# Optimization experiments

Hardware: AMD Instinct MI355X
Metric: run time of the kernel (lower is better)

Reference implementation:

```python
import jax, jax.numpy as jnp
import numpy as np

B, NM, MB, D = 16, 64, 64, 1024
NH, NKV, MEM = 16, 8, 64
HD = D // NH            # 64
S = MB + MEM            # per-step attention length
EPS = 1e-6

def precompute_freqs_cis(dim, end, theta=10000.0):
    freqs = 1.0 / (theta ** (jnp.arange(0, dim, 2)[: dim // 2].astype(jnp.float32) / dim))
    t = jnp.arange(end, dtype=jnp.float32)
    return jnp.exp(1j * jnp.outer(t, freqs))  # [end, dim//2] complex64

def apply_rope(x, fcis):
    # x: [s, h, d], fcis: [s, d//2] complex
    xc = x.reshape(x.shape[0], x.shape[1], HD // 2, 2)
    xc = jax.lax.complex(xc[..., 0], xc[..., 1]) * fcis[:, None, :]
    return jnp.stack([jnp.real(xc), jnp.imag(xc)], axis=-1).reshape(x.shape)

def layer_norm(x, scale, bias):
    m = x.mean(-1, keepdims=True)
    v = x.var(-1, keepdims=True)
    return (x - m) * jax.lax.rsqrt(v + EPS) * scale + bias

def setup_inputs() -> dict:
    key = jax.random.key(0)
    ks = jax.random.split(key, 8)
    s = 1.0 / np.sqrt(D)
    return {
        'hidden_states': jax.random.normal(ks[0], (B, NM, MB, D), jnp.float32),
        'mask': jax.random.bernoulli(ks[1], 0.9, (B, NM)),
        'mem_state': jax.random.normal(ks[2], (MEM, D), jnp.float32) * s,
        'wq': jax.random.normal(ks[3], (D, D), jnp.float32) * s,
        'wk': jax.random.normal(ks[4], (D, NKV * HD), jnp.float32) * s,
        'wv': jax.random.normal(ks[5], (D, NKV * HD), jnp.float32) * s,
        'wo': jax.random.normal(ks[6], (D, D), jnp.float32) * s,
        'pre_scale': jnp.ones((D,), jnp.float32),
        'pre_bias': jnp.zeros((D,), jnp.float32),
        'post_scale': jnp.ones((D,), jnp.float32),
        'post_bias': jnp.zeros((D,), jnp.float32),
    }

def reference(hidden_states, mask, mem_state, wq, wk, wv, wo, pre_scale, pre_bias, post_scale, post_bias):
    fcis = precompute_freqs_cis(HD, S)  # constant RoPE buffer, first S positions used
    rep = NH // NKV
    scale = 1.0 / np.sqrt(HD)

    def step(mem, inp):
        x_mb, m = inp  # x_mb: [MB, D], m: scalar bool
        h = layer_norm(jnp.concatenate([x_mb, mem], axis=0), pre_scale, pre_bias)  # [S, D]
        q = (h @ wq).reshape(S, NH, HD)
        k = (h @ wk).reshape(S, NKV, HD)
        v = (h @ wv).reshape(S, NKV, HD)
        q = apply_rope(q, fcis)
        k = apply_rope(k, fcis)
        k = jnp.repeat(k, rep, axis=1)  # GQA: expand kv heads
        v = jnp.repeat(v, rep, axis=1)
        qb, kb, vb = q.astype(jnp.bfloat16), k.astype(jnp.bfloat16), v.astype(jnp.bfloat16)
        logits = jnp.einsum('qhd,khd->hqk', qb, kb).astype(jnp.float32) * scale
        att = jax.nn.softmax(logits, axis=-1).astype(jnp.bfloat16)
        enc = jnp.einsum('hqk,khd->qhd', att, vb).reshape(S, D).astype(jnp.float32)
        out = enc[-MEM:] @ wo  # only memory-slot queries feed the update
        new_mem = layer_norm(out + mem, post_scale, post_bias)
        new_mem = jnp.where(m, new_mem, mem)  # lax.cond branch as select
        return new_mem, None

    def per_batch(x, m):
        final, _ = jax.lax.scan(step, mem_state, (x, m))
        return final

    return jax.vmap(per_batch)(hidden_states, mask)  # [B, MEM, D]
```

## Files before the change

### kernel.cpp

```cpp
#include <hip/hip_runtime.h>


typedef __attribute__((ext_vector_type(8))) _Float16 f16x8;
typedef __attribute__((ext_vector_type(4))) _Float16 f16x4;
typedef __attribute__((ext_vector_type(8))) short    s16x8;
typedef __attribute__((ext_vector_type(4))) float    f32x4;

#define NB   16
#define NMs  64
#define MBs  64
#define Dm   1024
#define NHh  16
#define NKVh 8
#define HDd  64
#define MEMm 64
#define Sq   128

__device__ __align__(16) _Float16      g_W1t[2048 * 1024];
__device__ __align__(16) _Float16      g_Wot[1024 * 1024];
__device__ __align__(16) float         g_rc[128 * 32];
__device__ __align__(16) float         g_rs[128 * 32];
__device__                unsigned char g_mask[NB * NMs];
__device__ __align__(16) _Float16      g_hx[(size_t)NB * NMs * MBs * Dm];
__device__ __align__(16) _Float16      g_hmem[NB * MEMm * Dm];
__device__ __align__(16) float         g_memA[NB * MEMm * Dm];
__device__ __align__(16) float         g_memB[NB * MEMm * Dm];
__device__ __align__(16) unsigned short g_qb[NB * NHh * 64 * 64];
__device__ __align__(16) unsigned short g_kb[NB * NKVh * 128 * 64];
__device__ __align__(16) unsigned short g_vt[NB * NKVh * 64 * 128];
__device__ __align__(16) _Float16      g_enc[NB * 64 * Dm];
__device__ __align__(16) float         g_outp[NB * 64 * Dm];

__device__ __forceinline__ unsigned short f2bf(float x) {
    union { float f; unsigned u; } v; v.f = x;
    unsigned u = v.u;
    return (unsigned short)((u + 0x7fffu + ((u >> 16) & 1u)) >> 16);
}
__device__ __forceinline__ float bf2f(unsigned short h) {
    union { unsigned u; float f; } v; v.u = ((unsigned)h) << 16; return v.f;
}

__device__ __forceinline__ void block_stats(float s, float ss, float eps,
                                            float* mean, float* rstd) {
    for (int off = 32; off > 0; off >>= 1) {
        s  += __shfl_down(s, off);
        ss += __shfl_down(ss, off);
    }
    __shared__ float red[8];
    int wid = threadIdx.x >> 6, lane = threadIdx.x & 63;
    __syncthreads();
    if (lane == 0) { red[wid] = s; red[4 + wid] = ss; }
    __syncthreads();
    float ts  = red[0] + red[1] + red[2] + red[3];
    float tss = red[4] + red[5] + red[6] + red[7];
    float m   = ts * (1.0f / 1024.0f);
    float var = tss * (1.0f / 1024.0f) - m * m;
    *mean = m;
    *rstd = rsqrtf(var + eps);
}

__global__ void k_transpose(const float* __restrict__ in, int ncols, int dsel) {
    _Float16* out = (dsel == 0) ? g_W1t
                  : (dsel == 1) ? (g_W1t + 1024 * 1024)
                  : (dsel == 2) ? (g_W1t + 1536 * 1024)
                                : g_Wot;
    __shared__ float tile[64][65];
    int bk = blockIdx.x, bn = blockIdx.y;
    int c = threadIdx.x & 63, rg = threadIdx.x >> 6;
    int k0 = bk * 64, n0 = bn * 64;
    for (int i = 0; i < 16; i++) {
        int r = rg * 16 + i;
        tile[r][c] = in[(size_t)(k0 + r) * ncols + n0 + c];
    }
    __syncthreads();
    for (int i = 0; i < 16; i++) {
        int r = rg * 16 + i;
        out[(size_t)(n0 + r) * 1024 + k0 + c] = (_Float16)tile[c][r];
    }
}

__global__ void k_rope() {
    int t = threadIdx.x;
    for (int j = 0; j < 32; j++) {
        double f = pow(10000.0, -(double)j / 32.0);
        double a = (double)t * f;
        g_rc[t * 32 + j] = (float)cos(a);
        g_rs[t * 32 + j] = (float)sin(a);
    }
}

__global__ void k_mask(const unsigned int* __restrict__ ip) {
    __shared__ int byteFmt;
    int t = threadIdx.x;
    if (t == 0) byteFmt = 0;
    __syncthreads();
    if (t < 256) {
        unsigned v = ip[t];
        if (!(v == 0u || v == 1u || v == 0x3F800000u)) byteFmt = 1;
    }
    __syncthreads();
    unsigned char m = byteFmt ? (((const unsigned char*)ip)[t] != 0)
                              : (ip[t] != 0u);
    g_mask[t] = m;
}

__global__ void k_ln_hx(const float* __restrict__ x,
                        const float* __restrict__ sc, const float* __restrict__ bi) {
    size_t row = blockIdx.x;
    int t = threadIdx.x;
    float4 v = ((const float4*)(x + row * 1024))[t];
    float mean, rstd;
    block_stats(v.x + v.y + v.z + v.w,
                v.x * v.x + v.y * v.y + v.z * v.z + v.w * v.w, 1e-6f, &mean, &rstd);
    float4 s4 = ((const float4*)sc)[t];
    float4 b4 = ((const float4*)bi)[t];
    f16x4 o;
    o[0] = (_Float16)((v.x - mean) * rstd * s4.x + b4.x);
    o[1] = (_Float16)((v.y - mean) * rstd * s4.y + b4.y);
    o[2] = (_Float16)((v.z - mean) * rstd * s4.z + b4.z);
    o[3] = (_Float16)((v.w - mean) * rstd * s4.w + b4.w);
    *(f16x4*)(g_hx + row * 1024 + t * 4) = o;
}

__global__ void k_ln_init(const float* __restrict__ ms,
                          const float* __restrict__ sc, const float* __restrict__ bi) {
    int b = blockIdx.x >> 6, r = blockIdx.x & 63;
    int t = threadIdx.x;
    float4 v = ((const float4*)(ms + (size_t)r * 1024))[t];
    ((float4*)(g_memA + ((size_t)b * 64 + r) * 1024))[t] = v;
    float mean, rstd;
    block_stats(v.x + v.y + v.z + v.w,
                v.x * v.x + v.y * v.y + v.z * v.z + v.w * v.w, 1e-6f, &mean, &rstd);
    float4 s4 = ((const float4*)sc)[t];
    float4 b4 = ((const float4*)bi)[t];
    f16x4 o;
    o[0] = (_Float16)((v.x - mean) * rstd * s4.x + b4.x);
    o[1] = (_Float16)((v.y - mean) * rstd * s4.y + b4.y);
    o[2] = (_Float16)((v.z - mean) * rstd * s4.z + b4.z);
    o[3] = (_Float16)((v.w - mean) * rstd * s4.w + b4.w);
    *(f16x4*)(g_hmem + ((size_t)b * 64 + r) * 1024 + t * 4) = o;
}

__device__ __forceinline__ void gemm_core(const _Float16* __restrict__ Abase,
                                          const _Float16* __restrict__ Bbase,
                                          _Float16* As, _Float16* Bs,
                                          f32x4 acc[2][2]) {
    int tid = threadIdx.x;
    int w = tid >> 6, l = tid & 63;
    int mo = (w & 1) * 32, no = (w >> 1) * 32;
    int sr = tid >> 2, sk = (tid & 3) * 8;
    int fr = l & 15, fq = (l >> 4) * 8;
    for (int kt = 0; kt < 32; ++kt) {
        f16x8 av = *(const f16x8*)(Abase + (size_t)sr * 1024 + kt * 32 + sk);
        f16x8 bv = *(const f16x8*)(Bbase + (size_t)sr * 1024 + kt * 32 + sk);
        __syncthreads();
        *(f16x8*)&As[sr * 40 + sk] = av;
        *(f16x8*)&Bs[sr * 40 + sk] = bv;
        __syncthreads();
        f16x8 a0 = *(const f16x8*)&As[(mo + fr) * 40 + fq];
        f16x8 a1 = *(const f16x8*)&As[(mo + 16 + fr) * 40 + fq];
        f16x8 b0 = *(const f16x8*)&Bs[(no + fr) * 40 + fq];
        f16x8 b1 = *(const f16x8*)&Bs[(no + 16 + fr) * 40 + fq];
        acc[0][0] = __builtin_amdgcn_mfma_f32_16x16x32_f16(a0, b0, acc[0][0], 0, 0, 0);
        acc[0][1] = __builtin_amdgcn_mfma_f32_16x16x32_f16(a0, b1, acc[0][1], 0, 0, 0);
        acc[1][0] = __builtin_amdgcn_mfma_f32_16x16x32_f16(a1, b0, acc[1][0], 0, 0, 0);
        acc[1][1] = __builtin_amdgcn_mfma_f32_16x16x32_f16(a1, b1, acc[1][1], 0, 0, 0);
    }
}

__launch_bounds__(256)
__global__ void k_gemm1(int s) {
    int bid = blockIdx.x;
    int b = bid / 48, t48 = bid % 48;
    int mtile = (t48 < 16) ? 0 : 1;
    int ntile = (t48 < 16) ? (16 + t48) : (t48 - 16);
    const _Float16* Abase = (mtile == 0)
        ? (g_hx + ((size_t)(b * NMs + s) * 64) * 1024)
        : (g_hmem + (size_t)b * 64 * 1024);
    const _Float16* Bbase = g_W1t + (size_t)ntile * 64 * 1024;
    __shared__ __align__(16) _Float16 As[64 * 40];
    __shared__ __align__(16) _Float16 Bs[64 * 40];
    f32x4 acc[2][2] = {};
    gemm_core(Abase, Bbase, As, Bs, acc);

    int tid = threadIdx.x, w = tid >> 6, l = tid & 63;
    int mo = (w & 1) * 32, no = (w >> 1) * 32;
    int quad = l >> 4, col = l & 15;
    int m0 = mtile * 64 + mo;
    int n0 = ntile * 64 + no;
    for (int i = 0; i < 2; i++)
        for (int j = 0; j < 2; j++)
            for (int r = 0; r < 4; r++) {
                float val = acc[i][j][r];
                float p = __shfl_xor(val, 1);
                int m = m0 + i * 16 + quad * 4 + r;
                int n = n0 + j * 16 + col;
                int d = n & 63;
                if (ntile < 16) {
                    int jj = d >> 1;
                    float c = g_rc[m * 32 + jj], sn = g_rs[m * 32 + jj];
                    float o = (d & 1) ? (p * sn + val * c) : (val * c - p * sn);
                    g_qb[(((size_t)b * 16 + ntile) * 64 + (m - 64)) * 64 + d] = f2bf(o);
                } else if (ntile < 24) {
                    int kvh = ntile - 16;
                    int jj = d >> 1;
                    float c = g_rc[m * 32 + jj], sn = g_rs[m * 32 + jj];
                    float o = (d & 1) ? (p * sn + val * c) : (val * c - p * sn);
                    g_kb[(((size_t)b * 8 + kvh) * 128 + m) * 64 + d] = f2bf(o);
                } else {
                    int kvh = ntile - 24;
                    g_vt[(((size_t)b * 8 + kvh) * 64 + d) * 128 + m] = f2bf(val);
                }
            }
}

__launch_bounds__(256)
__global__ void k_attn() {
    int b = blockIdx.x >> 4, h = blockIdx.x & 15, kvh = h >> 1;
    int tid = threadIdx.x, w = tid >> 6, l = tid & 63;
    int fr = l & 15, fq = (l >> 4) * 8;
    const unsigned short* qp = g_qb + ((size_t)b * 16 + h) * 64 * 64;
    const unsigned short* kp = g_kb + ((size_t)b * 8 + kvh) * 128 * 64;
    const unsigned short* vp = g_vt + ((size_t)b * 8 + kvh) * 64 * 128;

    s16x8 aq0 = *(const s16x8*)(qp + (w * 16 + fr) * 64 + fq);
    s16x8 aq1 = *(const s16x8*)(qp + (w * 16 + fr) * 64 + 32 + fq);
    f32x4 sc[8];
    for (int nt = 0; nt < 8; nt++) {
        sc[nt] = (f32x4){0.f, 0.f, 0.f, 0.f};
        s16x8 kb0 = *(const s16x8*)(kp + (nt * 16 + fr) * 64 + fq);
        s16x8 kb1 = *(const s16x8*)(kp + (nt * 16 + fr) * 64 + 32 + fq);
        sc[nt] = __builtin_amdgcn_mfma_f32_16x16x32_bf16(aq0, kb0, sc[nt], 0, 0, 0);
        sc[nt] = __builtin_amdgcn_mfma_f32_16x16x32_bf16(aq1, kb1, sc[nt], 0, 0, 0);
    }
    float lv[8][4];
    for (int nt = 0; nt < 8; nt++)
        for (int r = 0; r < 4; r++)
            lv[nt][r] = bf2f(f2bf(sc[nt][r])) * 0.125f;

    int quad = l >> 4;
    __shared__ __align__(16) unsigned short att_s[64 * 136];
    for (int r = 0; r < 4; r++) {
        float mx = -1e30f;
        for (int nt = 0; nt < 8; nt++) mx = fmaxf(mx, lv[nt][r]);
        for (int off = 1; off < 16; off <<= 1) mx = fmaxf(mx, __shfl_xor(mx, off));
        float sm = 0.f;
        for (int nt = 0; nt < 8; nt++) { lv[nt][r] = expf(lv[nt][r] - mx); sm += lv[nt][r]; }
        for (int off = 1; off < 16; off <<= 1) sm += __shfl_xor(sm, off);
        float inv = 1.0f / sm;
        int row = w * 16 + quad * 4 + r;
        for (int nt = 0; nt < 8; nt++)
            att_s[row * 136 + nt * 16 + fr] = f2bf(lv[nt][r] * inv);
    }
    f32x4 o[4];
    for (int nt = 0; nt < 4; nt++) o[nt] = (f32x4){0.f, 0.f, 0.f, 0.f};
    for (int kt = 0; kt < 4; kt++) {
        s16x8 a = *(const s16x8*)&att_s[(w * 16 + fr) * 136 + kt * 32 + fq];
        for (int nt = 0; nt < 4; nt++) {
            s16x8 bv = *(const s16x8*)(vp + (nt * 16 + fr) * 128 + kt * 32 + fq);
            o[nt] = __builtin_amdgcn_mfma_f32_16x16x32_bf16(a, bv, o[nt], 0, 0, 0);
        }
    }
    for (int nt = 0; nt < 4; nt++)
        for (int r = 0; r < 4; r++) {
            int m = w * 16 + quad * 4 + r;
            int d = nt * 16 + fr;
            g_enc[((size_t)b * 64 + m) * 1024 + h * 64 + d] =
                (_Float16)bf2f(f2bf(o[nt][r]));
        }
}

__launch_bounds__(256)
__global__ void k_gemm2() {
    int b = blockIdx.x >> 4, ntile = blockIdx.x & 15;
    const _Float16* Abase = g_enc + (size_t)b * 64 * 1024;
    const _Float16* Bbase = g_Wot + (size_t)ntile * 64 * 1024;
    __shared__ __align__(16) _Float16 As[64 * 40];
    __shared__ __align__(16) _Float16 Bs[64 * 40];
    f32x4 acc[2][2] = {};
    gemm_core(Abase, Bbase, As, Bs, acc);

    int tid = threadIdx.x, w = tid >> 6, l = tid & 63;
    int mo = (w & 1) * 32, no = (w >> 1) * 32;
    int quad = l >> 4, col = l & 15;
    for (int i = 0; i < 2; i++)
        for (int j = 0; j < 2; j++)
            for (int r = 0; r < 4; r++) {
                int m = mo + i * 16 + quad * 4 + r;
                int n = ntile * 64 + no + j * 16 + col;
                g_outp[((size_t)b * 64 + m) * 1024 + n] = acc[i][j][r];
            }
}

__global__ void k_ln2(int s, float* __restrict__ dout,
                      const float* __restrict__ psc, const float* __restrict__ pbi,
                      const float* __restrict__ qsc, const float* __restrict__ qbi) {
    int b = blockIdx.x >> 6, r = blockIdx.x & 63;
    const float* memIn = (s & 1) ? g_memB : g_memA;
    float* memOut = (s == 63) ? dout : ((s & 1) ? g_memA : g_memB);
    int t = threadIdx.x;
    size_t row = (size_t)b * 64 + r;
    float4 ov = ((const float4*)(g_outp + row * 1024))[t];
    float4 mv = ((const float4*)(memIn + row * 1024))[t];
    float4 y = {ov.x + mv.x, ov.y + mv.y, ov.z + mv.z, ov.w + mv.w};
    float mean, rstd;
    block_stats(y.x + y.y + y.z + y.w,
                y.x * y.x + y.y * y.y + y.z * y.z + y.w * y.w, 1e-6f, &mean, &rstd);
    float4 s4 = ((const float4*)psc)[t];
    float4 b4 = ((const float4*)pbi)[t];
    float4 nm = {(y.x - mean) * rstd * s4.x + b4.x,
                 (y.y - mean) * rstd * s4.y + b4.y,
                 (y.z - mean) * rstd * s4.z + b4.z,
                 (y.w - mean) * rstd * s4.w + b4.w};
    int mk = g_mask[b * 64 + s];
    float4 sel = mk ? nm : mv;
    ((float4*)(memOut + row * 1024))[t] = sel;
    float m2, rs2;
    block_stats(sel.x + sel.y + sel.z + sel.w,
                sel.x * sel.x + sel.y * sel.y + sel.z * sel.z + sel.w * sel.w,
                1e-6f, &m2, &rs2);
    float4 c4 = ((const float4*)qsc)[t];
    float4 d4 = ((const float4*)qbi)[t];
    f16x4 o;
    o[0] = (_Float16)((sel.x - m2) * rs2 * c4.x + d4.x);
    o[1] = (_Float16)((sel.y - m2) * rs2 * c4.y + d4.y);
    o[2] = (_Float16)((sel.z - m2) * rs2 * c4.z + d4.z);
    o[3] = (_Float16)((sel.w - m2) * rs2 * c4.w + d4.w);
    *(f16x4*)(g_hmem + row * 1024 + t * 4) = o;
}

extern "C" void kernel_launch(void* const* d_in, const int* in_sizes, int n_in,
                              void* d_out, int out_size, void* d_ws, size_t ws_size,
                              hipStream_t stream) {
    (void)in_sizes; (void)n_in; (void)d_ws; (void)ws_size; (void)out_size;
    const float* hidden    = (const float*)d_in[0];
    const unsigned int* mk = (const unsigned int*)d_in[1];
    const float* mem_state = (const float*)d_in[2];
    const float* wq  = (const float*)d_in[3];
    const float* wk  = (const float*)d_in[4];
    const float* wv  = (const float*)d_in[5];
    const float* wo  = (const float*)d_in[6];
    const float* pre_s  = (const float*)d_in[7];
    const float* pre_b  = (const float*)d_in[8];
    const float* post_s = (const float*)d_in[9];
    const float* post_b = (const float*)d_in[10];
    float* out = (float*)d_out;

    k_transpose<<<dim3(16, 16), 256, 0, stream>>>(wq, 1024, 0);
    k_transpose<<<dim3(16, 8),  256, 0, stream>>>(wk, 512, 1);
    k_transpose<<<dim3(16, 8),  256, 0, stream>>>(wv, 512, 2);
    k_transpose<<<dim3(16, 16), 256, 0, stream>>>(wo, 1024, 3);
    k_rope<<<1, 128, 0, stream>>>();
    k_mask<<<1, 1024, 0, stream>>>(mk);
    k_ln_hx<<<NB * NMs * MBs, 256, 0, stream>>>(hidden, pre_s, pre_b);
    k_ln_init<<<NB * MEMm, 256, 0, stream>>>(mem_state, pre_s, pre_b);

    for (int s = 0; s < NMs; ++s) {
        k_gemm1<<<NB * 48, 256, 0, stream>>>(s);
        k_attn<<<NB * NHh, 256, 0, stream>>>();
        k_gemm2<<<NB * 16, 256, 0, stream>>>();
        k_ln2<<<NB * MEMm, 256, 0, stream>>>(s, out, post_s, post_b, pre_s, pre_b);
    }
}
```

Before: 4.094 ms.

## Precompute hidden-state K/V projections in one batched GEMM and fuse QKV projection with attention

```diff
diff --git a/kernel.cpp b/kernel.cpp
--- a/kernel.cpp
+++ b/kernel.cpp
@@ -14,7 +14,6 @@
 #define NKVh 8
 #define HDd  64
 #define MEMm 64
-#define Sq   128
 
 __device__ __align__(16) _Float16      g_W1t[2048 * 1024];
 __device__ __align__(16) _Float16      g_Wot[1024 * 1024];
@@ -25,9 +24,8 @@
 __device__ __align__(16) _Float16      g_hmem[NB * MEMm * Dm];
 __device__ __align__(16) float         g_memA[NB * MEMm * Dm];
 __device__ __align__(16) float         g_memB[NB * MEMm * Dm];
-__device__ __align__(16) unsigned short g_qb[NB * NHh * 64 * 64];
-__device__ __align__(16) unsigned short g_kb[NB * NKVh * 128 * 64];
-__device__ __align__(16) unsigned short g_vt[NB * NKVh * 64 * 128];
+__device__ __align__(16) unsigned short g_kx[(size_t)NMs * NB * NKVh * 64 * 64];
+__device__ __align__(16) unsigned short g_vx[(size_t)NMs * NB * NKVh * 64 * 64];
 __device__ __align__(16) _Float16      g_enc[NB * 64 * Dm];
 __device__ __align__(16) float         g_outp[NB * 64 * Dm];
 
@@ -38,6 +36,12 @@
 }
 __device__ __forceinline__ float bf2f(unsigned short h) {
     union { unsigned u; float f; } v; v.u = ((unsigned)h) << 16; return v.f;
+}
+
+__device__ __forceinline__ void gload_lds16(const void* g, void* l) {
+    __builtin_amdgcn_global_load_lds(
+        (const __attribute__((address_space(1))) unsigned int*)g,
+        (__attribute__((address_space(3))) unsigned int*)l, 16, 0, 0);
 }
 
 __device__ __forceinline__ void block_stats(float s, float ss, float eps,
@@ -141,127 +145,219 @@
     *(f16x4*)(g_hmem + ((size_t)b * 64 + r) * 1024 + t * 4) = o;
 }
 
-__device__ __forceinline__ void gemm_core(const _Float16* __restrict__ Abase,
-                                          const _Float16* __restrict__ Bbase,
-                                          _Float16* As, _Float16* Bs,
-                                          f32x4 acc[2][2]) {
-    int tid = threadIdx.x;
-    int w = tid >> 6, l = tid & 63;
-    int mo = (w & 1) * 32, no = (w >> 1) * 32;
-    int sr = tid >> 2, sk = (tid & 3) * 8;
-    int fr = l & 15, fq = (l >> 4) * 8;
+__launch_bounds__(256)
+__global__ void k_kvx() {
+    int tm = blockIdx.x, tn = blockIdx.y;
+    int tid = threadIdx.x, w = tid >> 6, l = tid & 63;
+    int fr = l & 15, kc = l >> 4;
+    __shared__ __align__(16) _Float16 As[8 * 512];
+    __shared__ __align__(16) _Float16 Bs[8 * 512];
+    __shared__ __align__(16) unsigned short Ct[128 * 132];
+    const _Float16* A = g_hx + (size_t)tm * 128 * 1024;
+    const _Float16* B = g_W1t + (size_t)(1024 + tn * 128) * 1024;
+    int wm = w & 1, wn = w >> 1;
+    f32x4 acc[4][4];
+    #pragma unroll
+    for (int i = 0; i < 4; i++)
+        #pragma unroll
+        for (int j = 0; j < 4; j++) acc[i][j] = (f32x4){0.f, 0.f, 0.f, 0.f};
+
     for (int kt = 0; kt < 32; ++kt) {
-        f16x8 av = *(const f16x8*)(Abase + (size_t)sr * 1024 + kt * 32 + sk);
-        f16x8 bv = *(const f16x8*)(Bbase + (size_t)sr * 1024 + kt * 32 + sk);
-        __syncthreads();
-        *(f16x8*)&As[sr * 40 + sk] = av;
-        *(f16x8*)&Bs[sr * 40 + sk] = bv;
-        __syncthreads();
-        f16x8 a0 = *(const f16x8*)&As[(mo + fr) * 40 + fq];
-        f16x8 a1 = *(const f16x8*)&As[(mo + 16 + fr) * 40 + fq];
-        f16x8 b0 = *(const f16x8*)&Bs[(no + fr) * 40 + fq];
-        f16x8 b1 = *(const f16x8*)&Bs[(no + 16 + fr) * 40 + fq];
-        acc[0][0] = __builtin_amdgcn_mfma_f32_16x16x32_f16(a0, b0, acc[0][0], 0, 0, 0);
-        acc[0][1] = __builtin_amdgcn_mfma_f32_16x16x32_f16(a0, b1, acc[0][1], 0, 0, 0);
-        acc[1][0] = __builtin_amdgcn_mfma_f32_16x16x32_f16(a1, b0, acc[1][0], 0, 0, 0);
-        acc[1][1] = __builtin_amdgcn_mfma_f32_16x16x32_f16(a1, b1, acc[1][1], 0, 0, 0);
-    }
-}
-
-__launch_bounds__(256)
-__global__ void k_gemm1(int s) {
-    int bid = blockIdx.x;
-    int b = bid / 48, t48 = bid % 48;
-    int mtile = (t48 < 16) ? 0 : 1;
-    int ntile = (t48 < 16) ? (16 + t48) : (t48 - 16);
-    const _Float16* Abase = (mtile == 0)
-        ? (g_hx + ((size_t)(b * NMs + s) * 64) * 1024)
-        : (g_hmem + (size_t)b * 64 * 1024);
-    const _Float16* Bbase = g_W1t + (size_t)ntile * 64 * 1024;
-    __shared__ __align__(16) _Float16 As[64 * 40];
-    __shared__ __align__(16) _Float16 Bs[64 * 40];
-    f32x4 acc[2][2] = {};
-    gemm_core(Abase, Bbase, As, Bs, acc);
-
-    int tid = threadIdx.x, w = tid >> 6, l = tid & 63;
-    int mo = (w & 1) * 32, no = (w >> 1) * 32;
-    int quad = l >> 4, col = l & 15;
-    int m0 = mtile * 64 + mo;
-    int n0 = ntile * 64 + no;
-    for (int i = 0; i < 2; i++)
-        for (int j = 0; j < 2; j++)
+        #pragma unroll
+        for (int jj = 0; jj < 2; ++jj) {
+            int rg = w * 2 + jj;
+            gload_lds16(A + (size_t)(rg * 16 + fr) * 1024 + kt * 32 + kc * 8,
+                        (char*)As + rg * 1024);
+            gload_lds16(B + (size_t)(rg * 16 + fr) * 1024 + kt * 32 + kc * 8,
+                        (char*)Bs + rg * 1024);
+        }
+        __syncthreads();
+        f16x8 af[4], bg[4];
+        #pragma unroll
+        for (int i = 0; i < 4; i++) {
+            af[i] = *(const f16x8*)&As[(wm * 4 + i) * 512 + kc * 128 + fr * 8];
+            bg[i] = *(const f16x8*)&Bs[(wn * 4 + i) * 512 + kc * 128 + fr * 8];
+        }
+        #pragma unroll
+        for (int i = 0; i < 4; i++)
+            #pragma unroll
+            for (int j = 0; j < 4; j++)
+                acc[i][j] = __builtin_amdgcn_mfma_f32_16x16x32_f16(af[i], bg[j], acc[i][j], 0, 0, 0);
+        __syncthreads();
+    }
+    int quad = kc;
+    #pragma unroll
+    for (int i = 0; i < 4; i++)
+        #pragma unroll
+        for (int j = 0; j < 4; j++)
+            #pragma unroll
             for (int r = 0; r < 4; r++) {
                 float val = acc[i][j][r];
                 float p = __shfl_xor(val, 1);
-                int m = m0 + i * 16 + quad * 4 + r;
-                int n = n0 + j * 16 + col;
-                int d = n & 63;
-                if (ntile < 16) {
-                    int jj = d >> 1;
-                    float c = g_rc[m * 32 + jj], sn = g_rs[m * 32 + jj];
-                    float o = (d & 1) ? (p * sn + val * c) : (val * c - p * sn);
-                    g_qb[(((size_t)b * 16 + ntile) * 64 + (m - 64)) * 64 + d] = f2bf(o);
-                } else if (ntile < 24) {
-                    int kvh = ntile - 16;
-                    int jj = d >> 1;
-                    float c = g_rc[m * 32 + jj], sn = g_rs[m * 32 + jj];
-                    float o = (d & 1) ? (p * sn + val * c) : (val * c - p * sn);
-                    g_kb[(((size_t)b * 8 + kvh) * 128 + m) * 64 + d] = f2bf(o);
+                int rl = wm * 64 + i * 16 + quad * 4 + r;
+                int cl = wn * 64 + j * 16 + fr;
+                int c = tn * 128 + cl;
+                unsigned short ob;
+                if (c < 512) {
+                    int d = c & 63, pos = rl & 63;
+                    int j2 = d >> 1;
+                    float cc = g_rc[pos * 32 + j2], sn = g_rs[pos * 32 + j2];
+                    float o = (d & 1) ? (p * sn + val * cc) : (val * cc - p * sn);
+                    ob = f2bf(o);
                 } else {
-                    int kvh = ntile - 24;
-                    g_vt[(((size_t)b * 8 + kvh) * 64 + d) * 128 + m] = f2bf(val);
+                    ob = f2bf(val);
                 }
+                Ct[rl * 132 + cl] = ob;
             }
+    __syncthreads();
+    int row = tid >> 1, half = tid & 1;
+    size_t R = (size_t)tm * 128 + row;
+    int bb = (int)(R >> 12), ss = (int)((R >> 6) & 63), pos = (int)(R & 63);
+    int cb = tn * 128 + half * 64;
+    unsigned short* dst = (cb < 512)
+        ? (g_kx + ((((size_t)ss * 16 + bb) * 8) + (cb >> 6)) * 4096 + pos * 64)
+        : (g_vx + ((((size_t)ss * 16 + bb) * 8) + ((cb - 512) >> 6)) * 4096 + pos * 64);
+    const ushort4* src = (const ushort4*)&Ct[row * 132 + half * 64];
+    #pragma unroll
+    for (int j = 0; j < 16; j++) ((ushort4*)dst)[j] = src[j];
 }
 
 __launch_bounds__(256)
-__global__ void k_attn() {
+__global__ void k_step1(int s) {
     int b = blockIdx.x >> 4, h = blockIdx.x & 15, kvh = h >> 1;
     int tid = threadIdx.x, w = tid >> 6, l = tid & 63;
-    int fr = l & 15, fq = (l >> 4) * 8;
-    const unsigned short* qp = g_qb + ((size_t)b * 16 + h) * 64 * 64;
-    const unsigned short* kp = g_kb + ((size_t)b * 8 + kvh) * 128 * 64;
-    const unsigned short* vp = g_vt + ((size_t)b * 8 + kvh) * 64 * 128;
-
-    s16x8 aq0 = *(const s16x8*)(qp + (w * 16 + fr) * 64 + fq);
-    s16x8 aq1 = *(const s16x8*)(qp + (w * 16 + fr) * 64 + 32 + fq);
+    int fr = l & 15, kc = l >> 4, quad = kc;
+    __shared__ __align__(16) _Float16       Bs[24 * 512];
+    __shared__ __align__(16) unsigned short q_s[64 * 72];
+    __shared__ __align__(16) unsigned short k_s[64 * 72];
+    __shared__ __align__(16) unsigned short vt_s[64 * 136];
+    __shared__ __align__(16) unsigned short p_s[4][16 * 136];
+
+    const _Float16* A = g_hmem + (size_t)b * 64 * 1024;
+
+    {
+        const unsigned short* vx = g_vx + (((size_t)s * 16 + b) * 8 + kvh) * 4096;
+        int pos = tid & 63, dg = tid >> 6;
+        const ushort2* src = (const ushort2*)(vx + pos * 64 + dg * 16);
+        ushort2 tmp[8];
+        #pragma unroll
+        for (int j = 0; j < 8; j++) tmp[j] = src[j];
+        #pragma unroll
+        for (int j = 0; j < 8; j++) {
+            vt_s[(dg * 16 + 2 * j)     * 136 + pos] = tmp[j].x;
+            vt_s[(dg * 16 + 2 * j + 1) * 136 + pos] = tmp[j].y;
+        }
+    }
+
+    f32x4 acc[12];
+    #pragma unroll
+    for (int i = 0; i < 12; i++) acc[i] = (f32x4){0.f, 0.f, 0.f, 0.f};
+    int browQ = h * 64, browK = 1024 + kvh * 64, browV = 1536 + kvh * 64;
+
+    for (int kt = 0; kt < 16; ++kt) {
+        #pragma unroll
+        for (int jj = 0; jj < 6; ++jj) {
+            int m = w * 6 + jj, rg = m % 12, khalf = m / 12;
+            int r192 = rg * 16 + fr;
+            int brow = (r192 < 64) ? (browQ + r192)
+                     : (r192 < 128) ? (browK + r192 - 64)
+                                    : (browV + r192 - 128);
+            gload_lds16(g_W1t + (size_t)brow * 1024 + kt * 64 + khalf * 32 + kc * 8,
+                        (char*)Bs + m * 1024);
+        }
+        f16x8 a0 = *(const f16x8*)(A + (size_t)(w * 16 + fr) * 1024 + kt * 64 + kc * 8);
+        f16x8 a1 = *(const f16x8*)(A + (size_t)(w * 16 + fr) * 1024 + kt * 64 + 32 + kc * 8);
+        __syncthreads();
+        #pragma unroll
+        for (int nt = 0; nt < 12; ++nt) {
+            f16x8 b0 = *(const f16x8*)&Bs[nt * 512 + kc * 128 + fr * 8];
+            f16x8 b1 = *(const f16x8*)&Bs[(12 + nt) * 512 + kc * 128 + fr * 8];
+            acc[nt] = __builtin_amdgcn_mfma_f32_16x16x32_f16(a0, b0, acc[nt], 0, 0, 0);
+            acc[nt] = __builtin_amdgcn_mfma_f32_16x16x32_f16(a1, b1, acc[nt], 0, 0, 0);
+        }
+        __syncthreads();
+    }
+
+    #pragma unroll
+    for (int nt = 0; nt < 12; ++nt)
+        #pragma unroll
+        for (int r = 0; r < 4; ++r) {
+            float val = acc[nt][r];
+            float p = __shfl_xor(val, 1);
+            int row = w * 16 + quad * 4 + r;
+            int col = nt * 16 + fr;
+            if (col < 128) {
+                int d = col & 63, pos = 64 + row;
+                int j2 = d >> 1;
+                float cc = g_rc[pos * 32 + j2], sn = g_rs[pos * 32 + j2];
+                float o = (d & 1) ? (p * sn + val * cc) : (val * cc - p * sn);
+                unsigned short bo = f2bf(o);
+                if (col < 64) q_s[row * 72 + d] = bo;
+                else          k_s[row * 72 + d] = bo;
+            } else {
+                int d = col - 128;
+                vt_s[d * 136 + 64 + row] = f2bf(val);
+            }
+        }
+    __syncthreads();
+
+    s16x8 qa0 = *(const s16x8*)&q_s[(w * 16 + fr) * 72 + kc * 8];
+    s16x8 qa1 = *(const s16x8*)&q_s[(w * 16 + fr) * 72 + 32 + kc * 8];
+    const unsigned short* kx = g_kx + (((size_t)s * 16 + b) * 8 + kvh) * 4096;
     f32x4 sc[8];
-    for (int nt = 0; nt < 8; nt++) {
+    #pragma unroll
+    for (int nt = 0; nt < 8; ++nt) {
         sc[nt] = (f32x4){0.f, 0.f, 0.f, 0.f};
-        s16x8 kb0 = *(const s16x8*)(kp + (nt * 16 + fr) * 64 + fq);
-        s16x8 kb1 = *(const s16x8*)(kp + (nt * 16 + fr) * 64 + 32 + fq);
-        sc[nt] = __builtin_amdgcn_mfma_f32_16x16x32_bf16(aq0, kb0, sc[nt], 0, 0, 0);
-        sc[nt] = __builtin_amdgcn_mfma_f32_16x16x32_bf16(aq1, kb1, sc[nt], 0, 0, 0);
-    }
+        s16x8 kb0, kb1;
+        if (nt < 4) {
+            kb0 = *(const s16x8*)(kx + (nt * 16 + fr) * 64 + kc * 8);
+            kb1 = *(const s16x8*)(kx + (nt * 16 + fr) * 64 + 32 + kc * 8);
+        } else {
+            kb0 = *(const s16x8*)&k_s[((nt - 4) * 16 + fr) * 72 + kc * 8];
+            kb1 = *(const s16x8*)&k_s[((nt - 4) * 16 + fr) * 72 + 32 + kc * 8];
+        }
+        sc[nt] = __builtin_amdgcn_mfma_f32_16x16x32_bf16(qa0, kb0, sc[nt], 0, 0, 0);
+        sc[nt] = __builtin_amdgcn_mfma_f32_16x16x32_bf16(qa1, kb1, sc[nt], 0, 0, 0);
+    }
+
     float lv[8][4];
+    #pragma unroll
     for (int nt = 0; nt < 8; nt++)
+        #pragma unroll
         for (int r = 0; r < 4; r++)
             lv[nt][r] = bf2f(f2bf(sc[nt][r])) * 0.125f;
-
-    int quad = l >> 4;
-    __shared__ __align__(16) unsigned short att_s[64 * 136];
+    #pragma unroll
     for (int r = 0; r < 4; r++) {
         float mx = -1e30f;
+        #pragma unroll
         for (int nt = 0; nt < 8; nt++) mx = fmaxf(mx, lv[nt][r]);
         for (int off = 1; off < 16; off <<= 1) mx = fmaxf(mx, __shfl_xor(mx, off));
         float sm = 0.f;
+        #pragma unroll
         for (int nt = 0; nt < 8; nt++) { lv[nt][r] = expf(lv[nt][r] - mx); sm += lv[nt][r]; }
         for (int off = 1; off < 16; off <<= 1) sm += __shfl_xor(sm, off);
         float inv = 1.0f / sm;
-        int row = w * 16 + quad * 4 + r;
+        int row = quad * 4 + r;
+        #pragma unroll
         for (int nt = 0; nt < 8; nt++)
-            att_s[row * 136 + nt * 16 + fr] = f2bf(lv[nt][r] * inv);
-    }
+            p_s[w][row * 136 + nt * 16 + fr] = f2bf(lv[nt][r] * inv);
+    }
+    __syncthreads();
+
     f32x4 o[4];
+    #pragma unroll
     for (int nt = 0; nt < 4; nt++) o[nt] = (f32x4){0.f, 0.f, 0.f, 0.f};
-    for (int kt = 0; kt < 4; kt++) {
-        s16x8 a = *(const s16x8*)&att_s[(w * 16 + fr) * 136 + kt * 32 + fq];
-        for (int nt = 0; nt < 4; nt++) {
-            s16x8 bv = *(const s16x8*)(vp + (nt * 16 + fr) * 128 + kt * 32 + fq);
-            o[nt] = __builtin_amdgcn_mfma_f32_16x16x32_bf16(a, bv, o[nt], 0, 0, 0);
-        }
-    }
+    for (int kt2 = 0; kt2 < 4; ++kt2) {
+        s16x8 pa = *(const s16x8*)&p_s[w][fr * 136 + kt2 * 32 + kc * 8];
+        #pragma unroll
+        for (int nt = 0; nt < 4; ++nt) {
+            s16x8 vb = *(const s16x8*)&vt_s[(nt * 16 + fr) * 136 + kt2 * 32 + kc * 8];
+            o[nt] = __builtin_amdgcn_mfma_f32_16x16x32_bf16(pa, vb, o[nt], 0, 0, 0);
+        }
+    }
+    #pragma unroll
     for (int nt = 0; nt < 4; nt++)
+        #pragma unroll
         for (int r = 0; r < 4; r++) {
             int m = w * 16 + quad * 4 + r;
             int d = nt * 16 + fr;
@@ -272,24 +368,40 @@
 
 __launch_bounds__(256)
 __global__ void k_gemm2() {
-    int b = blockIdx.x >> 4, ntile = blockIdx.x & 15;
-    const _Float16* Abase = g_enc + (size_t)b * 64 * 1024;
-    const _Float16* Bbase = g_Wot + (size_t)ntile * 64 * 1024;
-    __shared__ __align__(16) _Float16 As[64 * 40];
-    __shared__ __align__(16) _Float16 Bs[64 * 40];
-    f32x4 acc[2][2] = {};
-    gemm_core(Abase, Bbase, As, Bs, acc);
-
+    int b = blockIdx.x >> 4, nt4 = blockIdx.x & 15;
     int tid = threadIdx.x, w = tid >> 6, l = tid & 63;
-    int mo = (w & 1) * 32, no = (w >> 1) * 32;
-    int quad = l >> 4, col = l & 15;
-    for (int i = 0; i < 2; i++)
-        for (int j = 0; j < 2; j++)
-            for (int r = 0; r < 4; r++) {
-                int m = mo + i * 16 + quad * 4 + r;
-                int n = ntile * 64 + no + j * 16 + col;
-                g_outp[((size_t)b * 64 + m) * 1024 + n] = acc[i][j][r];
-            }
+    int fr = l & 15, kc = l >> 4, quad = kc;
+    __shared__ __align__(16) _Float16 Bs[8 * 512];
+    const _Float16* A = g_enc + (size_t)b * 64 * 1024;
+    const _Float16* B = g_Wot + (size_t)nt4 * 64 * 1024;
+    f32x4 acc[4];
+    #pragma unroll
+    for (int i = 0; i < 4; i++) acc[i] = (f32x4){0.f, 0.f, 0.f, 0.f};
+    for (int kt = 0; kt < 16; ++kt) {
+        #pragma unroll
+        for (int jj = 0; jj < 2; ++jj) {
+            int m = w * 2 + jj, rg = m & 3, khalf = m >> 2;
+            gload_lds16(B + (size_t)(rg * 16 + fr) * 1024 + kt * 64 + khalf * 32 + kc * 8,
+                        (char*)Bs + m * 1024);
+        }
+        f16x8 a0 = *(const f16x8*)(A + (size_t)(w * 16 + fr) * 1024 + kt * 64 + kc * 8);
+        f16x8 a1 = *(const f16x8*)(A + (size_t)(w * 16 + fr) * 1024 + kt * 64 + 32 + kc * 8);
+        __syncthreads();
+        #pragma unroll
+        for (int nt = 0; nt < 4; ++nt) {
+            f16x8 b0 = *(const f16x8*)&Bs[nt * 512 + kc * 128 + fr * 8];
+            f16x8 b1 = *(const f16x8*)&Bs[(4 + nt) * 512 + kc * 128 + fr * 8];
+            acc[nt] = __builtin_amdgcn_mfma_f32_16x16x32_f16(a0, b0, acc[nt], 0, 0, 0);
+            acc[nt] = __builtin_amdgcn_mfma_f32_16x16x32_f16(a1, b1, acc[nt], 0, 0, 0);
+        }
+        __syncthreads();
+    }
+    #pragma unroll
+    for (int nt = 0; nt < 4; nt++)
+        #pragma unroll
+        for (int r = 0; r < 4; r++)
+            g_outp[((size_t)b * 64 + w * 16 + quad * 4 + r) * 1024 + nt4 * 64 + nt * 16 + fr]
+                = acc[nt][r];
 }
 
 __global__ void k_ln2(int s, float* __restrict__ dout,
@@ -354,11 +466,11 @@
     k_mask<<<1, 1024, 0, stream>>>(mk);
     k_ln_hx<<<NB * NMs * MBs, 256, 0, stream>>>(hidden, pre_s, pre_b);
     k_ln_init<<<NB * MEMm, 256, 0, stream>>>(mem_state, pre_s, pre_b);
+    k_kvx<<<dim3(512, 8), 256, 0, stream>>>();
 
     for (int s = 0; s < NMs; ++s) {
-        k_gemm1<<<NB * 48, 256, 0, stream>>>(s);
-        k_attn<<<NB * NHh, 256, 0, stream>>>();
-        k_gemm2<<<NB * 16, 256, 0, stream>>>();
+        k_step1<<<NB * NHh, 256, 0, stream>>>(s);
+        k_gemm2<<<NB * NHh, 256, 0, stream>>>();
         k_ln2<<<NB * MEMm, 256, 0, stream>>>(s, out, post_s, post_b, pre_s, pre_b);
     }
 }
```

Result: slower. 4.604 ms (+12.5%).
